# Optimization experiments

Hardware: AMD Instinct MI355X
Metric: run time of the kernel (lower is better)

The kernel has to match this reference:

```python
import jax, jax.numpy as jnp
import numpy as np


def setup_inputs() -> dict:
    key = jax.random.key(0)
    k1, k2 = jax.random.split(key)
    feat1 = jax.random.normal(k1, (4, 256, 64, 64), dtype=jnp.float32)
    feat2 = jax.random.normal(k2, (4, 256, 64, 64), dtype=jnp.float32)
    return {"feat1": feat1, "feat2": feat2}


def reference(feat1, feat2):
    b, c, h, w = feat1.shape
    hw = h * w
    f1 = feat1.reshape(b, c, hw)  # (b, c, hw)
    f2 = feat2.reshape(b, c, hw)  # (b, c, hw)
    # all-pairs dot-product correlation: corr[b, i, j] = sum_c f1[b,c,i] * f2[b,c,j]
    corr = jnp.einsum('bci,bcj->bij', f1, f2)  # (b, hw, hw)
    # softmax over query-position axis i (torch dim=1)
    out = jax.nn.softmax(corr, axis=1)
    return out.reshape(b, hw, h, w)
```

## Files before the change

### kernel.cpp

```cpp
#include <hip/hip_runtime.h>
#include <math.h>

#define HW 4096
#define NC 256
#define NB 4
#define NT 32

#define BM 128
#define BN 128
#define BK 32
#define LDP 40

typedef _Float16 f16;
typedef _Float16 half8 __attribute__((ext_vector_type(8)));
typedef float f32x4 __attribute__((ext_vector_type(4)));

__global__ __launch_bounds__(256) void gemm_corr_mfma(const float* __restrict__ f1,
                                                      const float* __restrict__ f2,
                                                      float* __restrict__ corr,
                                                      float* __restrict__ pm,
                                                      float* __restrict__ ps) {
    const int i0 = blockIdx.x * BM;
    const int j0 = blockIdx.y * BN;
    const int b  = blockIdx.z;
    const float* Ap = f1 + (size_t)b * NC * HW;
    const float* Bp = f2 + (size_t)b * NC * HW;
    float* Cp = corr + (size_t)b * HW * HW;

    __shared__ __align__(16) f16 Ash[BM * LDP];
    __shared__ __align__(16) f16 Asl[BM * LDP];
    __shared__ __align__(16) f16 Bsh[BN * LDP];
    __shared__ __align__(16) f16 Bsl[BN * LDP];

    const int t    = threadIdx.x;
    const int lane = t & 63;
    const int wave = t >> 6;
    const int wr   = (wave >> 1) * 64;
    const int wc   = (wave & 1) * 64;

    const int si  = t & 127;
    const int sc0 = (t >> 7) * 16;

    const int fm = lane & 15;
    const int fq = (lane >> 4) * 8;

    f32x4 acc[4][4];
#pragma unroll
    for (int u = 0; u < 4; ++u)
#pragma unroll
        for (int v = 0; v < 4; ++v) acc[u][v] = (f32x4)(0.f);

    for (int k0 = 0; k0 < NC; k0 += BK) {
        float av[16], bv[16];
#pragma unroll
        for (int q = 0; q < 16; ++q) {
            const size_t roff = (size_t)(k0 + sc0 + q) * HW;
            av[q] = Ap[roff + i0 + si];
            bv[q] = Bp[roff + j0 + si];
        }
        f16 ah[16], al[16], bh[16], bl[16];
#pragma unroll
        for (int q = 0; q < 16; ++q) {
            ah[q] = (f16)av[q];  al[q] = (f16)(av[q] - (float)ah[q]);
            bh[q] = (f16)bv[q];  bl[q] = (f16)(bv[q] - (float)bh[q]);
        }
        __syncthreads();
        const int wbase = si * LDP + sc0;
        *(half8*)&Ash[wbase]     = *(half8*)&ah[0];
        *(half8*)&Ash[wbase + 8] = *(half8*)&ah[8];
        *(half8*)&Asl[wbase]     = *(half8*)&al[0];
        *(half8*)&Asl[wbase + 8] = *(half8*)&al[8];
        *(half8*)&Bsh[wbase]     = *(half8*)&bh[0];
        *(half8*)&Bsh[wbase + 8] = *(half8*)&bh[8];
        *(half8*)&Bsl[wbase]     = *(half8*)&bl[0];
        *(half8*)&Bsl[wbase + 8] = *(half8*)&bl[8];
        __syncthreads();

        half8 fah[4], fal[4], fbh[4], fbl[4];
#pragma unroll
        for (int u = 0; u < 4; ++u) {
            const int ar = (wr + u * 16 + fm) * LDP + fq;
            fah[u] = *(const half8*)&Ash[ar];
            fal[u] = *(const half8*)&Asl[ar];
        }
#pragma unroll
        for (int v = 0; v < 4; ++v) {
            const int br = (wc + v * 16 + fm) * LDP + fq;
            fbh[v] = *(const half8*)&Bsh[br];
            fbl[v] = *(const half8*)&Bsl[br];
        }
#pragma unroll
        for (int u = 0; u < 4; ++u)
#pragma unroll
            for (int v = 0; v < 4; ++v) {
                acc[u][v] = __builtin_amdgcn_mfma_f32_16x16x32_f16(fah[u], fbh[v], acc[u][v], 0, 0, 0);
                acc[u][v] = __builtin_amdgcn_mfma_f32_16x16x32_f16(fah[u], fbl[v], acc[u][v], 0, 0, 0);
                acc[u][v] = __builtin_amdgcn_mfma_f32_16x16x32_f16(fal[u], fbh[v], acc[u][v], 0, 0, 0);
            }
    }

    __syncthreads();
    float* wred = (float*)Ash;

    float mcolv[4];
#pragma unroll
    for (int v = 0; v < 4; ++v) {
        float m16 = -INFINITY;
#pragma unroll
        for (int u = 0; u < 4; ++u)
#pragma unroll
            for (int r = 0; r < 4; ++r) m16 = fmaxf(m16, acc[u][v][r]);
        m16 = fmaxf(m16, __shfl_xor(m16, 16));
        m16 = fmaxf(m16, __shfl_xor(m16, 32));
        if ((lane >> 4) == 0) wred[wave * 64 + v * 16 + fm] = m16;
    }
    __syncthreads();

    const int widx = t >> 6;
    float stat_m = 0.f;
    if (t < BN) stat_m = fmaxf(wred[widx * 64 + (t & 63)],
                               wred[(widx + 2) * 64 + (t & 63)]);
#pragma unroll
    for (int v = 0; v < 4; ++v)
        mcolv[v] = fmaxf(wred[(wave & 1) * 64 + v * 16 + fm],
                         wred[((wave & 1) + 2) * 64 + v * 16 + fm]);
    __syncthreads();

    const int q4 = (lane >> 4) * 4;
#pragma unroll
    for (int v = 0; v < 4; ++v) {
        const int jj = j0 + wc + v * 16 + fm;
        float s16 = 0.f;
#pragma unroll
        for (int u = 0; u < 4; ++u) {
#pragma unroll
            for (int r = 0; r < 4; ++r) {
                const int ii = i0 + wr + u * 16 + q4 + r;
                const float p = __expf(acc[u][v][r] - mcolv[v]);
                Cp[(size_t)ii * HW + jj] = p;
                s16 += p;
            }
        }
        s16 += __shfl_xor(s16, 16);
        s16 += __shfl_xor(s16, 32);
        if ((lane >> 4) == 0) wred[wave * 64 + v * 16 + fm] = s16;
    }
    __syncthreads();

    if (t < BN) {
        const float s = wred[widx * 64 + (t & 63)] + wred[(widx + 2) * 64 + (t & 63)];
        const int sidx = blockIdx.x * (NB * HW) + b * HW + j0 + t;
        pm[sidx] = stat_m;
        ps[sidx] = s;
    }
}

__global__ __launch_bounds__(256) void softmax_combine(const float* __restrict__ pm,
                                                       const float* __restrict__ ps,
                                                       float* __restrict__ alpha) {
    const int idx = blockIdx.x * 256 + threadIdx.x;
    float pmv[NT], psv[NT], ec[NT];
    float m = -INFINITY;
#pragma unroll
    for (int c = 0; c < NT; ++c) {
        pmv[c] = pm[c * (NB * HW) + idx];
        psv[c] = ps[c * (NB * HW) + idx];
        m = fmaxf(m, pmv[c]);
    }
    float S = 0.f;
#pragma unroll
    for (int c = 0; c < NT; ++c) {
        ec[c] = __expf(pmv[c] - m);
        S += psv[c] * ec[c];
    }
    const float r = 1.0f / S;
#pragma unroll
    for (int c = 0; c < NT; ++c) alpha[c * (NB * HW) + idx] = ec[c] * r;
}

__global__ __launch_bounds__(256) void softmax_scale(float* __restrict__ corr,
                                                     const float* __restrict__ alpha) {
    const size_t base = ((size_t)blockIdx.x * 256 + threadIdx.x) * 4;
    const int b = (int)(base >> 24);
    const int i = ((int)(base >> 12)) & (HW - 1);
    const int j = ((int)base) & (HW - 1);
    const float4 a = *(const float4*)&alpha[(size_t)(i >> 7) * (NB * HW) + b * HW + j];
    float4 x = *(float4*)&corr[base];
    x.x *= a.x; x.y *= a.y; x.z *= a.z; x.w *= a.w;
    *(float4*)&corr[base] = x;
}

extern "C" void kernel_launch(void* const* d_in, const int* in_sizes, int n_in,
                              void* d_out, int out_size, void* d_ws, size_t ws_size,
                              hipStream_t stream) {
    const float* f1 = (const float*)d_in[0];
    const float* f2 = (const float*)d_in[1];
    float* out = (float*)d_out;

    float* pm = (float*)d_ws;
    float* ps = pm + NT * NB * HW;
    float* alpha = ps + NT * NB * HW;

    gemm_corr_mfma<<<dim3(HW / BM, HW / BN, NB), 256, 0, stream>>>(f1, f2, out, pm, ps);
    softmax_combine<<<NB * HW / 256, 256, 0, stream>>>(pm, ps, alpha);
    softmax_scale<<<(NB * (size_t)HW * HW) / (4 * 256), 256, 0, stream>>>(out, alpha);
}
```

Baseline: 565.8 us.

## Pre-split inputs into swizzled fp16 hi/lo tiles and load via global_load_lds

```diff
diff --git a/kernel.cpp b/kernel.cpp
--- a/kernel.cpp
+++ b/kernel.cpp
@@ -1,5 +1,6 @@
 #include <hip/hip_runtime.h>
 #include <math.h>
+#include <stdint.h>
 
 #define HW 4096
 #define NC 256
@@ -15,11 +16,193 @@
 typedef _Float16 half8 __attribute__((ext_vector_type(8)));
 typedef float f32x4 __attribute__((ext_vector_type(4)));
 
-__global__ __launch_bounds__(256) void gemm_corr_mfma(const float* __restrict__ f1,
-                                                      const float* __restrict__ f2,
-                                                      float* __restrict__ corr,
-                                                      float* __restrict__ pm,
-                                                      float* __restrict__ ps) {
+#define GLD16(gp, lp) __builtin_amdgcn_global_load_lds( \
+    (const __attribute__((address_space(1))) void*)(gp), \
+    (__attribute__((address_space(3))) void*)(lp), 16, 0, 0)
+
+__global__ __launch_bounds__(256) void split_tile(const float* __restrict__ src,
+                                                  f16* __restrict__ dh,
+                                                  f16* __restrict__ dl) {
+    const int it = blockIdx.x;
+    const int kt = blockIdx.y;
+    const int b  = blockIdx.z;
+    const float* S = src + (size_t)b * NC * HW + (size_t)kt * 32 * HW + it * 128;
+
+    __shared__ float st[32][133];
+    const int t = threadIdx.x;
+
+    {
+        const int i4 = (t & 31) * 4;
+        const int c0 = t >> 5;
+#pragma unroll
+        for (int p = 0; p < 4; ++p) {
+            const int c = c0 + p * 8;
+            const float4 v = *(const float4*)&S[(size_t)c * HW + i4];
+            st[c][i4] = v.x; st[c][i4 + 1] = v.y;
+            st[c][i4 + 2] = v.z; st[c][i4 + 3] = v.w;
+        }
+    }
+    __syncthreads();
+
+    const size_t tile_base = ((size_t)b * 256 + (size_t)it * 8 + kt) * (128 * 32);
+#pragma unroll
+    for (int p = 0; p < 2; ++p) {
+        const int cid = t + p * 256;
+        const int r = cid >> 2, ch = cid & 3;
+        f16 h8[8], l8[8];
+#pragma unroll
+        for (int q = 0; q < 8; ++q) {
+            const float x = st[ch * 8 + q][r];
+            h8[q] = (f16)x;
+            l8[q] = (f16)(x - (float)h8[q]);
+        }
+        const int off = r * 32 + ((ch ^ ((r >> 1) & 3)) << 3);
+        *(half8*)&dh[tile_base + off] = *(half8*)&h8[0];
+        *(half8*)&dl[tile_base + off] = *(half8*)&l8[0];
+    }
+}
+
+__global__ __launch_bounds__(256) void gemm_corr_mfma_t(const f16* __restrict__ Ah,
+                                                        const f16* __restrict__ Al,
+                                                        const f16* __restrict__ Bh,
+                                                        const f16* __restrict__ Bl,
+                                                        float* __restrict__ corr,
+                                                        float* __restrict__ pm,
+                                                        float* __restrict__ ps) {
+    const int it = blockIdx.x;
+    const int jt = blockIdx.y;
+    const int b  = blockIdx.z;
+    const int i0 = it * BM;
+    const int j0 = jt * BN;
+    float* Cp = corr + (size_t)b * HW * HW;
+
+    __shared__ __align__(16) f16 sAh[4096];
+    __shared__ __align__(16) f16 sAl[4096];
+    __shared__ __align__(16) f16 sBh[4096];
+    __shared__ __align__(16) f16 sBl[4096];
+
+    const int t    = threadIdx.x;
+    const int lane = t & 63;
+    const int wave = t >> 6;
+    const int wr   = (wave >> 1) * 64;
+    const int wc   = (wave & 1) * 64;
+    const int fm   = lane & 15;
+    const int ca   = lane >> 4;
+
+    const size_t abase = ((size_t)b * 256 + (size_t)it * 8) * 4096;
+    const size_t bbase = ((size_t)b * 256 + (size_t)jt * 8) * 4096;
+
+    const int swz = (fm >> 1) & 3;
+    const int cswz = ((ca ^ swz) << 3);
+    int aoff[4], boff[4];
+#pragma unroll
+    for (int u = 0; u < 4; ++u) aoff[u] = (wr + u * 16 + fm) * 32 + cswz;
+#pragma unroll
+    for (int v = 0; v < 4; ++v) boff[v] = (wc + v * 16 + fm) * 32 + cswz;
+
+    f32x4 acc[4][4];
+#pragma unroll
+    for (int u = 0; u < 4; ++u)
+#pragma unroll
+        for (int v = 0; v < 4; ++v) acc[u][v] = (f32x4)(0.f);
+
+    const int stg = (wave * 2) * 512 + lane * 8;
+    for (int kt = 0; kt < NC / BK; ++kt) {
+        __syncthreads();
+        const size_t koff = (size_t)kt * 4096;
+#pragma unroll
+        for (int p = 0; p < 2; ++p) {
+            const int h = stg + p * 512;
+            const int lb = (wave * 2 + p) * 512;
+            GLD16(Ah + abase + koff + h, &sAh[lb]);
+            GLD16(Al + abase + koff + h, &sAl[lb]);
+            GLD16(Bh + bbase + koff + h, &sBh[lb]);
+            GLD16(Bl + bbase + koff + h, &sBl[lb]);
+        }
+        __syncthreads();
+
+        half8 fah[4], fal[4], fbh[4], fbl[4];
+#pragma unroll
+        for (int u = 0; u < 4; ++u) {
+            fah[u] = *(const half8*)&sAh[aoff[u]];
+            fal[u] = *(const half8*)&sAl[aoff[u]];
+        }
+#pragma unroll
+        for (int v = 0; v < 4; ++v) {
+            fbh[v] = *(const half8*)&sBh[boff[v]];
+            fbl[v] = *(const half8*)&sBl[boff[v]];
+        }
+#pragma unroll
+        for (int u = 0; u < 4; ++u)
+#pragma unroll
+            for (int v = 0; v < 4; ++v) {
+                acc[u][v] = __builtin_amdgcn_mfma_f32_16x16x32_f16(fah[u], fbh[v], acc[u][v], 0, 0, 0);
+                acc[u][v] = __builtin_amdgcn_mfma_f32_16x16x32_f16(fah[u], fbl[v], acc[u][v], 0, 0, 0);
+                acc[u][v] = __builtin_amdgcn_mfma_f32_16x16x32_f16(fal[u], fbh[v], acc[u][v], 0, 0, 0);
+            }
+    }
+
+    __syncthreads();
+    float* wred = (float*)sAh;
+
+    float mcolv[4];
+#pragma unroll
+    for (int v = 0; v < 4; ++v) {
+        float m16 = -INFINITY;
+#pragma unroll
+        for (int u = 0; u < 4; ++u)
+#pragma unroll
+            for (int r = 0; r < 4; ++r) m16 = fmaxf(m16, acc[u][v][r]);
+        m16 = fmaxf(m16, __shfl_xor(m16, 16));
+        m16 = fmaxf(m16, __shfl_xor(m16, 32));
+        if ((lane >> 4) == 0) wred[wave * 64 + v * 16 + fm] = m16;
+    }
+    __syncthreads();
+
+    const int widx = t >> 6;
+    float stat_m = 0.f;
+    if (t < BN) stat_m = fmaxf(wred[widx * 64 + (t & 63)],
+                               wred[(widx + 2) * 64 + (t & 63)]);
+#pragma unroll
+    for (int v = 0; v < 4; ++v)
+        mcolv[v] = fmaxf(wred[(wave & 1) * 64 + v * 16 + fm],
+                         wred[((wave & 1) + 2) * 64 + v * 16 + fm]);
+    __syncthreads();
+
+    const int q4 = (lane >> 4) * 4;
+#pragma unroll
+    for (int v = 0; v < 4; ++v) {
+        const int jj = j0 + wc + v * 16 + fm;
+        float s16 = 0.f;
+#pragma unroll
+        for (int u = 0; u < 4; ++u) {
+#pragma unroll
+            for (int r = 0; r < 4; ++r) {
+                const int ii = i0 + wr + u * 16 + q4 + r;
+                const float p = __expf(acc[u][v][r] - mcolv[v]);
+                Cp[(size_t)ii * HW + jj] = p;
+                s16 += p;
+            }
+        }
+        s16 += __shfl_xor(s16, 16);
+        s16 += __shfl_xor(s16, 32);
+        if ((lane >> 4) == 0) wred[wave * 64 + v * 16 + fm] = s16;
+    }
+    __syncthreads();
+
+    if (t < BN) {
+        const float s = wred[widx * 64 + (t & 63)] + wred[(widx + 2) * 64 + (t & 63)];
+        const int sidx = blockIdx.x * (NB * HW) + b * HW + j0 + t;
+        pm[sidx] = stat_m;
+        ps[sidx] = s;
+    }
+}
+
+__global__ __launch_bounds__(256) void gemm_corr_mfma_fb(const float* __restrict__ f1,
+                                                         const float* __restrict__ f2,
+                                                         float* __restrict__ corr,
+                                                         float* __restrict__ pm,
+                                                         float* __restrict__ ps) {
     const int i0 = blockIdx.x * BM;
     const int j0 = blockIdx.y * BN;
     const int b  = blockIdx.z;
@@ -37,10 +220,8 @@
     const int wave = t >> 6;
     const int wr   = (wave >> 1) * 64;
     const int wc   = (wave & 1) * 64;
-
     const int si  = t & 127;
     const int sc0 = (t >> 7) * 16;
-
     const int fm = lane & 15;
     const int fq = (lane >> 4) * 8;
 
@@ -120,10 +301,11 @@
     float stat_m = 0.f;
     if (t < BN) stat_m = fmaxf(wred[widx * 64 + (t & 63)],
                                wred[(widx + 2) * 64 + (t & 63)]);
+    float mcv[4];
 #pragma unroll
     for (int v = 0; v < 4; ++v)
-        mcolv[v] = fmaxf(wred[(wave & 1) * 64 + v * 16 + fm],
-                         wred[((wave & 1) + 2) * 64 + v * 16 + fm]);
+        mcv[v] = fmaxf(wred[(wave & 1) * 64 + v * 16 + fm],
+                       wred[((wave & 1) + 2) * 64 + v * 16 + fm]);
     __syncthreads();
 
     const int q4 = (lane >> 4) * 4;
@@ -136,7 +318,7 @@
 #pragma unroll
             for (int r = 0; r < 4; ++r) {
                 const int ii = i0 + wr + u * 16 + q4 + r;
-                const float p = __expf(acc[u][v][r] - mcolv[v]);
+                const float p = __expf(acc[u][v][r] - mcv[v]);
                 Cp[(size_t)ii * HW + jj] = p;
                 s16 += p;
             }
@@ -200,8 +382,23 @@
     float* pm = (float*)d_ws;
     float* ps = pm + NT * NB * HW;
     float* alpha = ps + NT * NB * HW;
-
-    gemm_corr_mfma<<<dim3(HW / BM, HW / BN, NB), 256, 0, stream>>>(f1, f2, out, pm, ps);
+    f16* tiles = (f16*)(alpha + NT * NB * HW);
+    const size_t tile_elems = (size_t)NB * 256 * 4096;
+    f16* Ah = tiles;
+    f16* Al = Ah + tile_elems;
+    f16* Bh = Al + tile_elems;
+    f16* Bl = Bh + tile_elems;
+    const size_t need = 3ull * NT * NB * HW * 4 + 4ull * tile_elems * 2;
+
+    if (ws_size >= need) {
+        split_tile<<<dim3(HW / BM, NC / BK, NB), 256, 0, stream>>>(f1, Ah, Al);
+        split_tile<<<dim3(HW / BM, NC / BK, NB), 256, 0, stream>>>(f2, Bh, Bl);
+        gemm_corr_mfma_t<<<dim3(HW / BM, HW / BN, NB), 256, 0, stream>>>(
+            Ah, Al, Bh, Bl, out, pm, ps);
+    } else {
+        gemm_corr_mfma_fb<<<dim3(HW / BM, HW / BN, NB), 256, 0, stream>>>(
+            f1, f2, out, pm, ps);
+    }
     softmax_combine<<<NB * HW / 256, 256, 0, stream>>>(pm, ps, alpha);
     softmax_scale<<<(NB * (size_t)HW * HW) / (4 * 256), 256, 0, stream>>>(out, alpha);
 }
```

After: 494.7 us. 12.6% less time.
